# Performance work log

Measured on AMD Instinct MI355X. Metric: run time of the kernel, lower is better.

## Reference

```python
import jax, jax.numpy as jnp
import numpy as np

L, D, H, DK, DFF = 6, 768, 12, 64, 3072
VOCAB, NUM_BUCKETS, MAX_DIST = 32128, 32, 128
B, S = 8, 512
NEG = -1e9


def t5_layer_norm(x, w, eps=1e-6):
    var = jnp.mean(jnp.square(x), axis=-1, keepdims=True)
    return w * x * jax.lax.rsqrt(var + eps)


def relative_position_bucket(rel, num_buckets=NUM_BUCKETS, max_distance=MAX_DIST):
    # bidirectional T5 bucketing
    nb = num_buckets // 2
    ret = (rel > 0).astype(jnp.int32) * nb
    n = jnp.abs(rel)
    max_exact = nb // 2
    is_small = n < max_exact
    logf = jnp.log(jnp.maximum(n, 1).astype(jnp.float32) / max_exact)
    val_large = max_exact + (logf / np.log(max_distance / max_exact) * (nb - max_exact)).astype(jnp.int32)
    val_large = jnp.minimum(val_large, nb - 1)
    return ret + jnp.where(is_small, n, val_large)


def setup_inputs() -> dict:
    key = jax.random.key(0)
    ks = jax.random.split(key, 9)
    w = 0.02  # weight scale for numeric stability over 6 blocks
    return {
        "input_ids": jax.random.randint(ks[0], (B, S), 0, VOCAB),
        "attention_mask": jnp.ones((B, S), jnp.float32),
        "embed_w": jax.random.normal(ks[1], (VOCAB, D), jnp.float32),
        "ln1_w": jnp.ones((L, D), jnp.float32),
        "q_w": jax.random.normal(ks[2], (L, H * DK, D), jnp.float32) * w,
        "k_w": jax.random.normal(ks[3], (L, H * DK, D), jnp.float32) * w,
        "v_w": jax.random.normal(ks[4], (L, H * DK, D), jnp.float32) * w,
        "rel_bias_w": jax.random.normal(ks[5], (NUM_BUCKETS, H), jnp.float32),
        "o_w": jax.random.normal(ks[6], (L, D, H * DK), jnp.float32) * w,
        "ln2_w": jnp.ones((L, D), jnp.float32),
        "wi_w": jax.random.normal(ks[7], (L, DFF, D), jnp.float32) * w,
        "wo_w": jax.random.normal(ks[8], (L, D, DFF), jnp.float32) * w,
        "final_ln_w": jnp.ones((D,), jnp.float32),
    }


def reference(input_ids, attention_mask, embed_w, ln1_w, q_w, k_w, v_w,
              rel_bias_w, o_w, ln2_w, wi_w, wo_w, final_ln_w):
    b, s = input_ids.shape
    h = embed_w[input_ids]  # [B,S,D]

    # position bias computed once (block 0 owns the table; shared by all blocks)
    pos = jnp.arange(s)
    rel = pos[None, :] - pos[:, None]  # memory - query, [S,S]
    bucket = relative_position_bucket(rel)
    pos_bias = rel_bias_w[bucket]  # [S,S,H]
    pos_bias = jnp.transpose(pos_bias, (2, 0, 1))[None]  # [1,H,S,S]
    ext_mask = (1.0 - attention_mask)[:, None, None, :] * NEG  # [B,1,1,S]
    bias = pos_bias + ext_mask  # [B,H,S,S]

    for l in range(L):
        # --- self-attention (T5: no 1/sqrt(d) scaling) ---
        x = t5_layer_norm(h, ln1_w[l])
        q = jnp.einsum('bsd,id->bsi', x, q_w[l]).reshape(b, s, H, DK).transpose(0, 2, 1, 3)
        k = jnp.einsum('bsd,id->bsi', x, k_w[l]).reshape(b, s, H, DK).transpose(0, 2, 1, 3)
        v = jnp.einsum('bsd,id->bsi', x, v_w[l]).reshape(b, s, H, DK).transpose(0, 2, 1, 3)
        scores = jnp.einsum('bhqd,bhkd->bhqk', q, k) + bias
        attn = jax.nn.softmax(scores, axis=-1)
        ctx = jnp.einsum('bhqk,bhkd->bhqd', attn, v)
        ctx = ctx.transpose(0, 2, 1, 3).reshape(b, s, H * DK)
        h = h + jnp.einsum('bsi,di->bsd', ctx, o_w[l])
        # --- ReLU FFN ---
        x = t5_layer_norm(h, ln2_w[l])
        ff = jax.nn.relu(jnp.einsum('bsd,fd->bsf', x, wi_w[l]))
        h = h + jnp.einsum('bsf,df->bsd', ff, wo_w[l])

    return t5_layer_norm(h, final_ln_w)
```

## Files before the change

### kernel.cpp

```cpp
#include <hip/hip_runtime.h>
#include <hip/hip_bf16.h>
#include <math.h>

#define L_ 6
#define D_ 768
#define H_ 12
#define DK_ 64
#define DFF_ 3072
#define NB_ 32
#define MAXDIST_ 128
#define B_ 8
#define S_ 512
#define NEG_ (-1e9f)
#define BS_ (B_*S_)
#define BSD_ ((size_t)BS_*D_)

typedef __bf16 bf16x8 __attribute__((ext_vector_type(8)));
typedef float f32x4 __attribute__((ext_vector_type(4)));

__device__ __forceinline__ unsigned short f2bf(float f) {
    unsigned u = __float_as_uint(f);
    u += 0x7fff + ((u >> 16) & 1);
    return (unsigned short)(u >> 16);
}
__device__ __forceinline__ float bf2f(unsigned short s) {
    return __uint_as_float(((unsigned)s) << 16);
}

#define GLDS(g, l) __builtin_amdgcn_global_load_lds( \
    (const __attribute__((address_space(1))) void*)(const void*)(g), \
    (__attribute__((address_space(3))) void*)(void*)(l), 16, 0, 0)

__global__ __launch_bounds__(192) void k_embed(const int* __restrict__ ids,
                                               const float* __restrict__ ew,
                                               float* __restrict__ h) {
    int row = blockIdx.x;
    int id = ids[row];
    const float4* src = (const float4*)(ew + (size_t)id * D_);
    float4* dst = (float4*)(h + (size_t)row * D_);
    dst[threadIdx.x] = src[threadIdx.x];
}

template<int OUTBF>
__global__ __launch_bounds__(256) void k_rmsnorm(const float* __restrict__ in,
                                                 const float* __restrict__ w,
                                                 void* __restrict__ outp) {
    int row = blockIdx.x;
    int tid = threadIdx.x;
    const float* x = in + (size_t)row * D_;
    float ss = 0.f;
    for (int i = tid; i < D_; i += 256) { float v = x[i]; ss += v * v; }
    #pragma unroll
    for (int off = 32; off; off >>= 1) ss += __shfl_down(ss, off, 64);
    __shared__ float sbuf[4];
    if ((tid & 63) == 0) sbuf[tid >> 6] = ss;
    __syncthreads();
    float tot = sbuf[0] + sbuf[1] + sbuf[2] + sbuf[3];
    float scale = rsqrtf(tot / (float)D_ + 1e-6f);
    if (OUTBF) {
        unsigned short* o = (unsigned short*)outp + (size_t)row * D_;
        for (int i = tid; i < D_; i += 256) o[i] = f2bf(w[i] * x[i] * scale);
    } else {
        float* o = (float*)outp + (size_t)row * D_;
        for (int i = tid; i < D_; i += 256) o[i] = w[i] * x[i] * scale;
    }
}

__global__ __launch_bounds__(256) void k_posbias(const float* __restrict__ rbw,
                                                 unsigned short* __restrict__ biasg) {
    int idx = blockIdx.x * 256 + threadIdx.x;
    if (idx >= S_ * S_) return;
    int q = idx / S_, key = idx - q * S_;
    int rel = key - q;
    const int nb = NB_ / 2;
    int ret = rel > 0 ? nb : 0;
    int n = rel < 0 ? -rel : rel;
    const int max_exact = nb / 2;
    int val;
    if (n < max_exact) {
        val = n;
    } else {
        float lf = logf((float)n / (float)max_exact) /
                   logf((float)MAXDIST_ / (float)max_exact) * (float)(nb - max_exact);
        val = max_exact + (int)lf;
        if (val > nb - 1) val = nb - 1;
    }
    int bucket = ret + val;
    #pragma unroll
    for (int hh = 0; hh < H_; ++hh)
        biasg[((size_t)hh * S_ + q) * S_ + key] = f2bf(rbw[bucket * H_ + hh]);
}

#define W1V8 73728
#define W2V8 294912
__global__ __launch_bounds__(256) void k_wconv(const float* __restrict__ qw,
                                               const float* __restrict__ kw,
                                               const float* __restrict__ vw,
                                               const float* __restrict__ ow,
                                               const float* __restrict__ wiw,
                                               const float* __restrict__ wow,
                                               unsigned short* __restrict__ wb) {
    int gid = blockIdx.x * 256 + threadIdx.x;
    int i = gid;
    const float* src;
    if (i < W1V8)                src = qw;
    else if ((i -= W1V8) < W1V8) src = kw;
    else if ((i -= W1V8) < W1V8) src = vw;
    else if ((i -= W1V8) < W1V8) src = ow;
    else if ((i -= W1V8) < W2V8) src = wiw;
    else { i -= W2V8;            src = wow; }
    const float4* s4 = (const float4*)src + (size_t)i * 2;
    float4 a = s4[0], b = s4[1];
    ushort4 lo, hi;
    lo.x = f2bf(a.x); lo.y = f2bf(a.y); lo.z = f2bf(a.z); lo.w = f2bf(a.w);
    hi.x = f2bf(b.x); hi.y = f2bf(b.y); hi.z = f2bf(b.z); hi.w = f2bf(b.w);
    ushort4* d = (ushort4*)(wb + (size_t)gid * 8);
    d[0] = lo; d[1] = hi;
}

template<int BM, int BN>
__device__ __forceinline__ void stage_tile_t(const unsigned short* __restrict__ Abase,
                                             const unsigned short* __restrict__ Bbase,
                                             int k0, int K, int buf,
                                             unsigned short* lsA, unsigned short* lsB,
                                             int w, int lane) {
    constexpr int CA = BM / 32, CB = BN / 32;
    #pragma unroll
    for (int c = 0; c < CA; ++c) {
        int off = c * 4096 + w * 1024 + lane * 16;
        int row = off >> 7;
        int sc = (off & 127) ^ ((row & 7) << 4);
        GLDS(Abase + (size_t)row * K + k0 + (sc >> 1), (char*)lsA + buf * (BM * 128) + off);
    }
    #pragma unroll
    for (int c = 0; c < CB; ++c) {
        int off = c * 4096 + w * 1024 + lane * 16;
        int row = off >> 7;
        int sc = (off & 127) ^ ((row & 7) << 4);
        GLDS(Bbase + (size_t)row * K + k0 + (sc >> 1), (char*)lsB + buf * (BN * 128) + off);
    }
}

template<int BM, int BN>
__device__ __forceinline__ void gemm_compute_t(const char* cA, const char* cB,
                                               f32x4 acc[BM / 32][BN / 32],
                                               int l15, int l4, int wr, int wc) {
    constexpr int MI = BM / 32, NJ = BN / 32;
    #pragma unroll
    for (int kk = 0; kk < 2; ++kk) {
        bf16x8 af[MI], bfr[NJ];
        int kByte = kk * 64 + l4 * 16;
        #pragma unroll
        for (int i = 0; i < MI; ++i) {
            int r = wr + i * 16 + l15;
            af[i] = *(const bf16x8*)(cA + r * 128 + (kByte ^ ((r & 7) << 4)));
        }
        #pragma unroll
        for (int j = 0; j < NJ; ++j) {
            int r = wc + j * 16 + l15;
            bfr[j] = *(const bf16x8*)(cB + r * 128 + (kByte ^ ((r & 7) << 4)));
        }
        #pragma unroll
        for (int i = 0; i < MI; ++i)
            #pragma unroll
            for (int j = 0; j < NJ; ++j)
                acc[i][j] = __builtin_amdgcn_mfma_f32_16x16x32_bf16(af[i], bfr[j], acc[i][j], 0, 0, 0);
    }
}

template<int BM, int BN>
__device__ __forceinline__ void gemm_core_t(const unsigned short* __restrict__ A,
                                            const unsigned short* __restrict__ Bw,
                                            int K, int bm, int bn,
                                            unsigned short* lsA, unsigned short* lsB,
                                            f32x4 acc[BM / 32][BN / 32]) {
    int t = threadIdx.x, lane = t & 63, w = t >> 6;
    int l15 = lane & 15, l4 = lane >> 4;
    int wr = (w >> 1) * (BM / 2), wc = (w & 1) * (BN / 2);
    const unsigned short* Abase = A + (size_t)(bm * BM) * K;
    const unsigned short* Bbase = Bw + (size_t)(bn * BN) * K;
    int nt = K >> 6;

    stage_tile_t<BM, BN>(Abase, Bbase, 0, K, 0, lsA, lsB, w, lane);
    for (int tq = 0; tq < nt - 1; ++tq) {
        int cur = tq & 1;
        stage_tile_t<BM, BN>(Abase, Bbase, (tq + 1) << 6, K, cur ^ 1, lsA, lsB, w, lane);
        if constexpr (BM / 32 + BN / 32 == 8)
            asm volatile("s_waitcnt vmcnt(8)" ::: "memory");
        else
            asm volatile("s_waitcnt vmcnt(4)" ::: "memory");
        __builtin_amdgcn_s_barrier();
        gemm_compute_t<BM, BN>((const char*)lsA + cur * (BM * 128),
                               (const char*)lsB + cur * (BN * 128), acc, l15, l4, wr, wc);
        asm volatile("s_waitcnt lgkmcnt(0)" ::: "memory");
        __builtin_amdgcn_s_barrier();
    }
    int cur = (nt - 1) & 1;
    asm volatile("s_waitcnt vmcnt(0)" ::: "memory");
    __builtin_amdgcn_s_barrier();
    gemm_compute_t<BM, BN>((const char*)lsA + cur * (BM * 128),
                           (const char*)lsB + cur * (BN * 128), acc, l15, l4, wr, wc);
}

template<int BM, int BN, int RES, int RELU, int OUTBF>
__global__ __launch_bounds__(256) void k_gemm_t(const unsigned short* __restrict__ A,
                                                const unsigned short* __restrict__ Bw,
                                                const float* __restrict__ res,
                                                void* __restrict__ C, int N, int K) {
    __shared__ __align__(16) unsigned short lsA[2 * BM * 64];
    __shared__ __align__(16) unsigned short lsB[2 * BN * 64];
    f32x4 acc[BM / 32][BN / 32] = {};
    int bm = blockIdx.x, bn = blockIdx.y;
    gemm_core_t<BM, BN>(A, Bw, K, bm, bn, lsA, lsB, acc);
    int t = threadIdx.x, lane = t & 63, w = t >> 6;
    int l15 = lane & 15, l4 = lane >> 4;
    int wr = (w >> 1) * (BM / 2), wc = (w & 1) * (BN / 2);
    #pragma unroll
    for (int i = 0; i < BM / 32; ++i) {
        #pragma unroll
        for (int r = 0; r < 4; ++r) {
            int row = bm * BM + wr + i * 16 + l4 * 4 + r;
            #pragma unroll
            for (int j = 0; j < BN / 32; ++j) {
                int col = bn * BN + wc + j * 16 + l15;
                float v = acc[i][j][r];
                if (RES)  v += res[(size_t)row * N + col];
                if (RELU) v = fmaxf(v, 0.f);
                if (OUTBF) ((unsigned short*)C)[(size_t)row * N + col] = f2bf(v);
                else       ((float*)C)[(size_t)row * N + col] = v;
            }
        }
    }
}

__global__ __launch_bounds__(256) void k_gemm_qkv_bf(const unsigned short* __restrict__ X,
                                                     const unsigned short* __restrict__ wq,
                                                     const unsigned short* __restrict__ wk,
                                                     const unsigned short* __restrict__ wv,
                                                     unsigned short* __restrict__ qo,
                                                     unsigned short* __restrict__ ko,
                                                     unsigned short* __restrict__ vt) {
    __shared__ __align__(16) unsigned short lsA[2 * 128 * 64];
    __shared__ __align__(16) unsigned short lsB[2 * 128 * 64];
    f32x4 acc[4][4] = {};
    int z = blockIdx.z;
    const unsigned short* Bm = z == 0 ? wq : (z == 1 ? wk : wv);
    int bm = blockIdx.x, bn = blockIdx.y;
    gemm_core_t<128, 128>(X, Bm, D_, bm, bn, lsA, lsB, acc);
    int t = threadIdx.x, lane = t & 63, w = t >> 6;
    int l15 = lane & 15, l4 = lane >> 4;
    int wr = (w >> 1) * 64, wc = (w & 1) * 64;
    if (z < 2) {
        unsigned short* C = z == 0 ? qo : ko;
        #pragma unroll
        for (int i = 0; i < 4; ++i)
            #pragma unroll
            for (int r = 0; r < 4; ++r) {
                int row = bm * 128 + wr + i * 16 + l4 * 4 + r;
                #pragma unroll
                for (int j = 0; j < 4; ++j) {
                    int col = bn * 128 + wc + j * 16 + l15;
                    C[(size_t)row * D_ + col] = f2bf(acc[i][j][r]);
                }
            }
    } else {
        #pragma unroll
        for (int i = 0; i < 4; ++i) {
            int row0 = bm * 128 + wr + i * 16 + l4 * 4;
            int b = row0 >> 9, s0 = row0 & 511;
            #pragma unroll
            for (int j = 0; j < 4; ++j) {
                int col = bn * 128 + wc + j * 16 + l15;
                int hh = col >> 6, dv = col & 63;
                ushort4 o4;
                o4.x = f2bf(acc[i][j][0]); o4.y = f2bf(acc[i][j][1]);
                o4.z = f2bf(acc[i][j][2]); o4.w = f2bf(acc[i][j][3]);
                *(ushort4*)(vt + (((size_t)b * H_ + hh) * 64 + dv) * S_ + s0) = o4;
            }
        }
    }
}

__global__ __launch_bounds__(256) void k_attn_flash(const unsigned short* __restrict__ qb,
                                                    const unsigned short* __restrict__ kb,
                                                    const unsigned short* __restrict__ vtb,
                                                    const unsigned short* __restrict__ biasg,
                                                    const float* __restrict__ mask,
                                                    unsigned short* __restrict__ ctx) {
    __shared__ __align__(16) unsigned short Kt[64 * 64];
    __shared__ __align__(16) unsigned short Vt[64 * 64];
    __shared__ __align__(16) unsigned short Bt[64 * 64];
    __shared__ __align__(16) unsigned short Pt[4][16 * 64];

    int t = threadIdx.x, lane = t & 63, w = t >> 6;
    int l15 = lane & 15, l4 = lane >> 4;
    int bh = blockIdx.y;
    int b = bh / H_, hh = bh - b * H_;
    int qblk = blockIdx.x;
    int qloc = w * 16 + l15;
    int qg = qblk * 64 + qloc;

    bf16x8 qf[2];
    {
        const unsigned short* qp = qb + ((size_t)(b * S_ + qg)) * D_ + hh * DK_;
        qf[0] = *(const bf16x8*)(qp + l4 * 8);
        qf[1] = *(const bf16x8*)(qp + 32 + l4 * 8);
    }
    float mrun = -1e30f, lsum = 0.f;
    f32x4 cacc[4] = {};

    for (int kt = 0; kt < S_ / 64; ++kt) {
        int kbase = kt * 64;
        __syncthreads();
        #pragma unroll
        for (int c = 0; c < 2; ++c) {
            int off = (w * 2 + c) * 1024 + lane * 16;
            int row = off >> 7;
            int colb = (off & 127) ^ ((row & 7) << 4);
            GLDS(kb + ((size_t)(b * S_ + kbase + row)) * D_ + hh * DK_ + (colb >> 1),
                 (char*)Kt + off);
            GLDS(vtb + ((size_t)bh * 64 + row) * S_ + kbase + (colb >> 1),
                 (char*)Vt + off);
            GLDS(biasg + ((size_t)hh * S_ + qblk * 64 + row) * S_ + kbase + (colb >> 1),
                 (char*)Bt + off);
        }
        __syncthreads();

        f32x4 sc[4] = {};
        #pragma unroll
        for (int kk = 0; kk < 2; ++kk) {
            int kByte = kk * 64 + l4 * 16;
            #pragma unroll
            for (int j = 0; j < 4; ++j) {
                int r = j * 16 + l15;
                bf16x8 kf = *(const bf16x8*)((const char*)Kt + r * 128 + (kByte ^ ((r & 7) << 4)));
                sc[j] = __builtin_amdgcn_mfma_f32_16x16x32_bf16(kf, qf[kk], sc[j], 0, 0, 0);
            }
        }
        float sv[4][4];
        float tmax = -1e30f;
        #pragma unroll
        for (int j = 0; j < 4; ++j) {
            int bro = qloc * 128 + ((j * 32 + l4 * 8) ^ ((qloc & 7) << 4));
            ushort4 b4 = *(const ushort4*)((const char*)Bt + bro);
            float4 m4 = *(const float4*)(mask + (size_t)b * S_ + kbase + j * 16 + l4 * 4);
            sv[j][0] = sc[j][0] + bf2f(b4.x) + (1.f - m4.x) * NEG_;
            sv[j][1] = sc[j][1] + bf2f(b4.y) + (1.f - m4.y) * NEG_;
            sv[j][2] = sc[j][2] + bf2f(b4.z) + (1.f - m4.z) * NEG_;
            sv[j][3] = sc[j][3] + bf2f(b4.w) + (1.f - m4.w) * NEG_;
            tmax = fmaxf(tmax, fmaxf(fmaxf(sv[j][0], sv[j][1]), fmaxf(sv[j][2], sv[j][3])));
        }
        tmax = fmaxf(tmax, __shfl_xor(tmax, 16, 64));
        tmax = fmaxf(tmax, __shfl_xor(tmax, 32, 64));
        float mnew = fmaxf(mrun, tmax);
        float scal = __expf(mrun - mnew);
        #pragma unroll
        for (int i = 0; i < 4; ++i) {
            cacc[i][0] *= scal; cacc[i][1] *= scal;
            cacc[i][2] *= scal; cacc[i][3] *= scal;
        }
        float psum = 0.f;
        unsigned pp[8];
        #pragma unroll
        for (int j = 0; j < 4; ++j) {
            float p0 = __expf(sv[j][0] - mnew), p1 = __expf(sv[j][1] - mnew);
            float p2 = __expf(sv[j][2] - mnew), p3 = __expf(sv[j][3] - mnew);
            psum += (p0 + p1) + (p2 + p3);
            pp[j * 2]     = (unsigned)f2bf(p0) | ((unsigned)f2bf(p1) << 16);
            pp[j * 2 + 1] = (unsigned)f2bf(p2) | ((unsigned)f2bf(p3) << 16);
        }
        lsum = lsum * scal + psum;
        mrun = mnew;
        unsigned short* P = Pt[w];
        #pragma unroll
        for (int j = 0; j < 4; ++j) {
            int base = l15 * 128 + ((j * 32 + l4 * 8) ^ ((l15 & 7) << 4));
            *(unsigned*)((char*)P + base) = pp[j * 2];
            *(unsigned*)((char*)P + base + 4) = pp[j * 2 + 1];
        }
        #pragma unroll
        for (int kk = 0; kk < 2; ++kk) {
            int kByte = kk * 64 + l4 * 16;
            bf16x8 pf = *(const bf16x8*)((const char*)P + l15 * 128 + (kByte ^ ((l15 & 7) << 4)));
            #pragma unroll
            for (int i = 0; i < 4; ++i) {
                int rr = i * 16 + l15;
                bf16x8 vf = *(const bf16x8*)((const char*)Vt + rr * 128 + (kByte ^ ((rr & 7) << 4)));
                cacc[i] = __builtin_amdgcn_mfma_f32_16x16x32_bf16(vf, pf, cacc[i], 0, 0, 0);
            }
        }
    }
    lsum += __shfl_xor(lsum, 16, 64);
    lsum += __shfl_xor(lsum, 32, 64);
    float inv = 1.f / lsum;
    unsigned short* cp = ctx + ((size_t)(b * S_ + qg)) * D_ + hh * DK_;
    #pragma unroll
    for (int i = 0; i < 4; ++i) {
        ushort4 o4;
        o4.x = f2bf(cacc[i][0] * inv); o4.y = f2bf(cacc[i][1] * inv);
        o4.z = f2bf(cacc[i][2] * inv); o4.w = f2bf(cacc[i][3] * inv);
        *(ushort4*)(cp + i * 16 + l4 * 4) = o4;
    }
}

extern "C" void kernel_launch(void* const* d_in, const int* in_sizes, int n_in,
                              void* d_out, int out_size, void* d_ws, size_t ws_size,
                              hipStream_t stream) {
    const int*   ids  = (const int*)d_in[0];
    const float* mask = (const float*)d_in[1];
    const float* ew   = (const float*)d_in[2];
    const float* ln1  = (const float*)d_in[3];
    const float* qw   = (const float*)d_in[4];
    const float* kw   = (const float*)d_in[5];
    const float* vw   = (const float*)d_in[6];
    const float* rbw  = (const float*)d_in[7];
    const float* ow   = (const float*)d_in[8];
    const float* ln2  = (const float*)d_in[9];
    const float* wiw  = (const float*)d_in[10];
    const float* wow  = (const float*)d_in[11];
    const float* flnw = (const float*)d_in[12];
    float* out = (float*)d_out;

    char* p = (char*)d_ws;
    float* h = (float*)p;                        p += BSD_ * 4;
    unsigned short* biasg = (unsigned short*)p;  p += (size_t)H_ * S_ * S_ * 2;
    unsigned short* wbuf  = (unsigned short*)p;  p += (size_t)7077888 * 2;
    unsigned short* xbf   = (unsigned short*)p;  p += BSD_ * 2;
    unsigned short* ctxb  = xbf;
    unsigned short* qbB   = (unsigned short*)p;  p += BSD_ * 2;
    unsigned short* kbB   = (unsigned short*)p;  p += BSD_ * 2;
    unsigned short* vtb   = (unsigned short*)p;  p += BSD_ * 2;
                    p += BSD_ * 2;
    unsigned short* ff    = qbB;

    const unsigned short* wq  = wbuf;
    const unsigned short* wk  = wbuf + 589824;
    const unsigned short* wv  = wbuf + 1179648;
    const unsigned short* wo  = wbuf + 1769472;
    const unsigned short* wwi = wbuf + 2359296;
    const unsigned short* wwo = wbuf + 4718592;

    k_embed<<<BS_, 192, 0, stream>>>(ids, ew, h);
    k_posbias<<<(S_ * S_ + 255) / 256, 256, 0, stream>>>(rbw, biasg);

    for (int l = 0; l < L_; ++l) {
        k_wconv<<<3456, 256, 0, stream>>>(qw + (size_t)l * 589824, kw + (size_t)l * 589824,
                                          vw + (size_t)l * 589824, ow + (size_t)l * 589824,
                                          wiw + (size_t)l * 2359296, wow + (size_t)l * 2359296,
                                          wbuf);
        k_rmsnorm<1><<<BS_, 256, 0, stream>>>(h, ln1 + (size_t)l * D_, xbf);
        k_gemm_qkv_bf<<<dim3(BS_ / 128, D_ / 128, 3), 256, 0, stream>>>(
            xbf, wq, wk, wv, qbB, kbB, vtb);
        k_attn_flash<<<dim3(S_ / 64, B_ * H_), 256, 0, stream>>>(
            qbB, kbB, vtb, biasg, mask, ctxb);
        k_gemm_t<64, 64, 1, 0, 0><<<dim3(BS_ / 64, D_ / 64), 256, 0, stream>>>(
            ctxb, wo, h, h, D_, D_);
        k_rmsnorm<1><<<BS_, 256, 0, stream>>>(h, ln2 + (size_t)l * D_, xbf);
        k_gemm_t<128, 128, 0, 1, 1><<<dim3(BS_ / 128, DFF_ / 128), 256, 0, stream>>>(
            xbf, wwi, nullptr, ff, DFF_, D_);
        k_gemm_t<64, 64, 1, 0, 0><<<dim3(BS_ / 64, D_ / 64), 256, 0, stream>>>(
            ff, wwo, h, h, D_, DFF_);
    }
    k_rmsnorm<0><<<BS_, 256, 0, stream>>>(h, flnw, out);
}
```

Measured before the change: 935.8 us.

## Convert all layer weights in one launch and shrink QKV/FFN-in tiles to 64x128

Replaces the six per-layer weight-conversion launches with one kernel that converts all layers into a larger bf16 buffer, saving launches and serialization. It also changes the QKV and FFN-up GEMMs from 128x128 to 64x128 tiles, with a matching vmcnt wait for the 6-load staging case, to launch more workgroups on the many-CU GPU. The trade-off is a larger workspace and lower per-tile reuse in the GEMMs.

```diff
diff --git a/kernel.cpp b/kernel.cpp
--- a/kernel.cpp
+++ b/kernel.cpp
@@ -14,6 +14,7 @@
 #define NEG_ (-1e9f)
 #define BS_ (B_*S_)
 #define BSD_ ((size_t)BS_*D_)
+#define WLAYER_ 7077888
 
 typedef __bf16 bf16x8 __attribute__((ext_vector_type(8)));
 typedef float f32x4 __attribute__((ext_vector_type(4)));
@@ -93,22 +94,24 @@
 
 #define W1V8 73728
 #define W2V8 294912
-__global__ __launch_bounds__(256) void k_wconv(const float* __restrict__ qw,
-                                               const float* __restrict__ kw,
-                                               const float* __restrict__ vw,
-                                               const float* __restrict__ ow,
-                                               const float* __restrict__ wiw,
-                                               const float* __restrict__ wow,
-                                               unsigned short* __restrict__ wb) {
+#define WLV8 884736
+__global__ __launch_bounds__(256) void k_wconv_all(const float* __restrict__ qw,
+                                                   const float* __restrict__ kw,
+                                                   const float* __restrict__ vw,
+                                                   const float* __restrict__ ow,
+                                                   const float* __restrict__ wiw,
+                                                   const float* __restrict__ wow,
+                                                   unsigned short* __restrict__ wb) {
     int gid = blockIdx.x * 256 + threadIdx.x;
-    int i = gid;
+    int l = gid / WLV8;
+    int i = gid - l * WLV8;
     const float* src;
-    if (i < W1V8)                src = qw;
-    else if ((i -= W1V8) < W1V8) src = kw;
-    else if ((i -= W1V8) < W1V8) src = vw;
-    else if ((i -= W1V8) < W1V8) src = ow;
-    else if ((i -= W1V8) < W2V8) src = wiw;
-    else { i -= W2V8;            src = wow; }
+    if (i < W1V8)                src = qw  + (size_t)l * 589824;
+    else if ((i -= W1V8) < W1V8) src = kw  + (size_t)l * 589824;
+    else if ((i -= W1V8) < W1V8) src = vw  + (size_t)l * 589824;
+    else if ((i -= W1V8) < W1V8) src = ow  + (size_t)l * 589824;
+    else if ((i -= W1V8) < W2V8) src = wiw + (size_t)l * 2359296;
+    else { i -= W2V8;            src = wow + (size_t)l * 2359296; }
     const float4* s4 = (const float4*)src + (size_t)i * 2;
     float4 a = s4[0], b = s4[1];
     ushort4 lo, hi;
@@ -180,15 +183,15 @@
     const unsigned short* Abase = A + (size_t)(bm * BM) * K;
     const unsigned short* Bbase = Bw + (size_t)(bn * BN) * K;
     int nt = K >> 6;
+    constexpr int NL = BM / 32 + BN / 32;
 
     stage_tile_t<BM, BN>(Abase, Bbase, 0, K, 0, lsA, lsB, w, lane);
     for (int tq = 0; tq < nt - 1; ++tq) {
         int cur = tq & 1;
         stage_tile_t<BM, BN>(Abase, Bbase, (tq + 1) << 6, K, cur ^ 1, lsA, lsB, w, lane);
-        if constexpr (BM / 32 + BN / 32 == 8)
-            asm volatile("s_waitcnt vmcnt(8)" ::: "memory");
-        else
-            asm volatile("s_waitcnt vmcnt(4)" ::: "memory");
+        if constexpr (NL == 8)      asm volatile("s_waitcnt vmcnt(8)" ::: "memory");
+        else if constexpr (NL == 6) asm volatile("s_waitcnt vmcnt(6)" ::: "memory");
+        else                        asm volatile("s_waitcnt vmcnt(4)" ::: "memory");
         __builtin_amdgcn_s_barrier();
         gemm_compute_t<BM, BN>((const char*)lsA + cur * (BM * 128),
                                (const char*)lsB + cur * (BN * 128), acc, l15, l4, wr, wc);
@@ -240,23 +243,23 @@
                                                      unsigned short* __restrict__ qo,
                                                      unsigned short* __restrict__ ko,
                                                      unsigned short* __restrict__ vt) {
-    __shared__ __align__(16) unsigned short lsA[2 * 128 * 64];
+    __shared__ __align__(16) unsigned short lsA[2 * 64 * 64];
     __shared__ __align__(16) unsigned short lsB[2 * 128 * 64];
-    f32x4 acc[4][4] = {};
+    f32x4 acc[2][4] = {};
     int z = blockIdx.z;
     const unsigned short* Bm = z == 0 ? wq : (z == 1 ? wk : wv);
     int bm = blockIdx.x, bn = blockIdx.y;
-    gemm_core_t<128, 128>(X, Bm, D_, bm, bn, lsA, lsB, acc);
+    gemm_core_t<64, 128>(X, Bm, D_, bm, bn, lsA, lsB, acc);
     int t = threadIdx.x, lane = t & 63, w = t >> 6;
     int l15 = lane & 15, l4 = lane >> 4;
-    int wr = (w >> 1) * 64, wc = (w & 1) * 64;
+    int wr = (w >> 1) * 32, wc = (w & 1) * 64;
     if (z < 2) {
         unsigned short* C = z == 0 ? qo : ko;
         #pragma unroll
-        for (int i = 0; i < 4; ++i)
+        for (int i = 0; i < 2; ++i)
             #pragma unroll
             for (int r = 0; r < 4; ++r) {
-                int row = bm * 128 + wr + i * 16 + l4 * 4 + r;
+                int row = bm * 64 + wr + i * 16 + l4 * 4 + r;
                 #pragma unroll
                 for (int j = 0; j < 4; ++j) {
                     int col = bn * 128 + wc + j * 16 + l15;
@@ -265,8 +268,8 @@
             }
     } else {
         #pragma unroll
-        for (int i = 0; i < 4; ++i) {
-            int row0 = bm * 128 + wr + i * 16 + l4 * 4;
+        for (int i = 0; i < 2; ++i) {
+            int row0 = bm * 64 + wr + i * 16 + l4 * 4;
             int b = row0 >> 9, s0 = row0 & 511;
             #pragma unroll
             for (int j = 0; j < 4; ++j) {
@@ -424,7 +427,7 @@
     char* p = (char*)d_ws;
     float* h = (float*)p;                        p += BSD_ * 4;
     unsigned short* biasg = (unsigned short*)p;  p += (size_t)H_ * S_ * S_ * 2;
-    unsigned short* wbuf  = (unsigned short*)p;  p += (size_t)7077888 * 2;
+    unsigned short* wball = (unsigned short*)p;  p += (size_t)L_ * WLAYER_ * 2;
     unsigned short* xbf   = (unsigned short*)p;  p += BSD_ * 2;
     unsigned short* ctxb  = xbf;
     unsigned short* qbB   = (unsigned short*)p;  p += BSD_ * 2;
@@ -433,30 +436,28 @@
                     p += BSD_ * 2;
     unsigned short* ff    = qbB;
 
-    const unsigned short* wq  = wbuf;
-    const unsigned short* wk  = wbuf + 589824;
-    const unsigned short* wv  = wbuf + 1179648;
-    const unsigned short* wo  = wbuf + 1769472;
-    const unsigned short* wwi = wbuf + 2359296;
-    const unsigned short* wwo = wbuf + 4718592;
-
     k_embed<<<BS_, 192, 0, stream>>>(ids, ew, h);
     k_posbias<<<(S_ * S_ + 255) / 256, 256, 0, stream>>>(rbw, biasg);
+    k_wconv_all<<<(L_ * WLV8) / 256, 256, 0, stream>>>(qw, kw, vw, ow, wiw, wow, wball);
 
     for (int l = 0; l < L_; ++l) {
-        k_wconv<<<3456, 256, 0, stream>>>(qw + (size_t)l * 589824, kw + (size_t)l * 589824,
-                                          vw + (size_t)l * 589824, ow + (size_t)l * 589824,
-                                          wiw + (size_t)l * 2359296, wow + (size_t)l * 2359296,
-                                          wbuf);
+        const unsigned short* wl  = wball + (size_t)l * WLAYER_;
+        const unsigned short* wq  = wl;
+        const unsigned short* wk  = wl + 589824;
+        const unsigned short* wv  = wl + 1179648;
+        const unsigned short* wo  = wl + 1769472;
+        const unsigned short* wwi = wl + 2359296;
+        const unsigned short* wwo = wl + 4718592;
+
         k_rmsnorm<1><<<BS_, 256, 0, stream>>>(h, ln1 + (size_t)l * D_, xbf);
-        k_gemm_qkv_bf<<<dim3(BS_ / 128, D_ / 128, 3), 256, 0, stream>>>(
+        k_gemm_qkv_bf<<<dim3(BS_ / 64, D_ / 128, 3), 256, 0, stream>>>(
             xbf, wq, wk, wv, qbB, kbB, vtb);
         k_attn_flash<<<dim3(S_ / 64, B_ * H_), 256, 0, stream>>>(
             qbB, kbB, vtb, biasg, mask, ctxb);
         k_gemm_t<64, 64, 1, 0, 0><<<dim3(BS_ / 64, D_ / 64), 256, 0, stream>>>(
             ctxb, wo, h, h, D_, D_);
         k_rmsnorm<1><<<BS_, 256, 0, stream>>>(h, ln2 + (size_t)l * D_, xbf);
-        k_gemm_t<128, 128, 0, 1, 1><<<dim3(BS_ / 128, DFF_ / 128), 256, 0, stream>>>(
+        k_gemm_t<64, 128, 0, 1, 1><<<dim3(BS_ / 64, DFF_ / 128), 256, 0, stream>>>(
             xbf, wwi, nullptr, ff, DFF_, D_);
         k_gemm_t<64, 64, 1, 0, 0><<<dim3(BS_ / 64, D_ / 64), 256, 0, stream>>>(
             ff, wwo, h, h, D_, DFF_);
```

Result: faster. 879.0 us (-6.1%).
